# Performance work log

Measured on AMD Instinct MI355X. Metric: run time of the kernel, lower is better.

The kernel has to match this reference:

```python
import jax, jax.numpy as jnp
import numpy as np

VOCAB = 10000
EMB = 256
FILTERS = 256
KS = [2, 3, 4]
NUM_LABELS = 6
B, L = 4, 256


def _conv1d_same(x, w, b, k):
    # x: [B, C, L], w: [O, I, k] -> [B, O, L]; torch 'same' pad: left=(k-1)//2
    pad_l = (k - 1) // 2
    pad_r = (k - 1) - pad_l
    y = jax.lax.conv_general_dilated(
        x, w, window_strides=(1,), padding=[(pad_l, pad_r)],
        dimension_numbers=('NCH', 'OIH', 'NCH'))
    return y + b[None, :, None]


def setup_inputs() -> dict:
    key = jax.random.key(0)
    ks = jax.random.split(key, 12)
    s = 0.02
    return {
        'input_ids': jax.random.randint(ks[0], (B, L), 0, VOCAB),
        'emb_table': jax.random.normal(ks[1], (VOCAB, EMB), jnp.float32) * s,
        'w2': jax.random.normal(ks[2], (FILTERS, EMB, 2), jnp.float32) * s,
        'b2': jax.random.normal(ks[3], (FILTERS,), jnp.float32) * s,
        'w3': jax.random.normal(ks[4], (FILTERS, EMB, 3), jnp.float32) * s,
        'b3': jax.random.normal(ks[5], (FILTERS,), jnp.float32) * s,
        'w4': jax.random.normal(ks[6], (FILTERS, EMB, 4), jnp.float32) * s,
        'b4': jax.random.normal(ks[7], (FILTERS,), jnp.float32) * s,
        'triple_w': jax.random.normal(ks[8], (NUM_LABELS, 3 * FILTERS), jnp.float32) * s,
        'triple_b': jax.random.normal(ks[9], (NUM_LABELS,), jnp.float32) * s,
        'score_w': jax.random.normal(ks[10], (1, 3 * FILTERS), jnp.float32) * s,
        'score_b': jax.random.normal(ks[11], (1,), jnp.float32) * s,
    }


def reference(input_ids, emb_table, w2, b2, w3, b3, w4, b4,
              triple_w, triple_b, score_w, score_b):
    emb = emb_table[input_ids]              # [B, L, E]
    x = jnp.transpose(emb, (0, 2, 1))       # [B, E, L]
    outs = [_conv1d_same(x, w, b, k) for (w, b, k)
            in ((w2, b2, 2), (w3, b3, 3), (w4, b4, 4))]
    out = jnp.concatenate(outs, axis=1)     # [B, 3F, L]
    out = jnp.transpose(out, (0, 2, 1))     # [B, L, K], K = 3F
    # dropout is identity in eval mode
    pair = jnp.einsum('bik,bjk->bijk', out, out)          # [B, L, L, K]
    triple_logits = jnp.einsum('bijk,ck->bijc', pair, triple_w) + triple_b
    scores = jnp.einsum('bijk,ck->bijc', pair, score_w) + score_b
    scores = scores[..., 0]                 # squeeze(-1) -> [B, L, L]
    return triple_logits, scores
```

## Files before the change

kernel.cpp:

```cpp
#include <hip/hip_runtime.h>
#include <stdint.h>

#define LSEQ 256
#define EMB  256
#define K3F  768
#define SCOFF (4 * 256 * 256 * 6)

typedef short bf16x8 __attribute__((ext_vector_type(8)));
typedef float f32x4  __attribute__((ext_vector_type(4)));

__device__ __forceinline__ uint16_t f2bf(float x) {
    union { float f; uint32_t u; } c; c.f = x;
    uint32_t r = c.u + 0x7fffu + ((c.u >> 16) & 1u);
    return (uint16_t)(r >> 16);
}

__global__ __launch_bounds__(256) void k_prep(const int* __restrict__ ids,
                                              const float* __restrict__ table,
                                              const float* __restrict__ w2,
                                              const float* __restrict__ w3,
                                              const float* __restrict__ w4,
                                              uint16_t* __restrict__ embB,
                                              uint16_t* __restrict__ Wt2,
                                              uint16_t* __restrict__ Wt3,
                                              uint16_t* __restrict__ Wt4) {
    int blk = blockIdx.x, tid = threadIdx.x;
    if (blk < 32) {
        int b = blk >> 3, l0 = (blk & 7) << 5;
        int r = tid >> 3, p = tid & 7;
        int id = ids[(b << 8) + l0 + r];
        const float* src = table + (size_t)id * EMB + p * 32;
        uint16_t* dst = embB + (size_t)(b * 272 + 4 + l0 + r) * 256 + p * 32;
#pragma unroll
        for (int s = 0; s < 8; ++s) {
            float4 v = *(const float4*)(src + 4 * s);
            uint32_t lo = f2bf(v.x) | ((uint32_t)f2bf(v.y) << 16);
            uint32_t hi = f2bf(v.z) | ((uint32_t)f2bf(v.w) << 16);
            *(uint2*)(dst + 4 * s) = make_uint2(lo, hi);
        }
    } else if (blk < 36) {
        int b = blk - 32;
        int ri = tid >> 4;
        int row = ri < 4 ? ri : 256 + ri;
        int off = (tid & 15) * 16;
        uint16_t* dst = embB + (size_t)(b * 272 + row) * 256 + off;
        *(uint4*)dst = make_uint4(0, 0, 0, 0);
        *(uint4*)(dst + 8) = make_uint4(0, 0, 0, 0);
    } else {
        int n = (blk - 36) * 256 + tid;
        if (n < 65536) {
            int c = n >> 8, i = n & 255;
            float2 v = *(const float2*)(w2 + (c << 9) + (i << 1));
            Wt2[c * 256 + i]         = f2bf(v.x);
            Wt2[65536 + c * 256 + i] = f2bf(v.y);
        } else if (n < 131072) {
            int m = n - 65536;
            int c = m >> 8, i = m & 255;
            const float* s = w3 + c * 768 + i * 3;
#pragma unroll
            for (int t = 0; t < 3; ++t)
                Wt3[t * 65536 + c * 256 + i] = f2bf(s[t]);
        } else {
            int m = n - 131072;
            int c = m >> 8, i = m & 255;
            float4 v = *(const float4*)(w4 + (c << 10) + (i << 2));
            Wt4[c * 256 + i]              = f2bf(v.x);
            Wt4[65536 + c * 256 + i]      = f2bf(v.y);
            Wt4[2 * 65536 + c * 256 + i]  = f2bf(v.z);
            Wt4[3 * 65536 + c * 256 + i]  = f2bf(v.w);
        }
    }
}

template <int K, int PAD>
__device__ __forceinline__ void convg_body(const uint16_t* __restrict__ Wt,
                                           const float* __restrict__ bias,
                                           const uint16_t* __restrict__ embB,
                                           const float* __restrict__ tw,
                                           const float* __restrict__ sw,
                                           uint16_t* __restrict__ VB,
                                           uint16_t* __restrict__ U,
                                           int b, int c0, int l0, int gbase,
                                           uint16_t (*As)[32][72], uint16_t (*Bs)[72],
                                           float (*twb)[32]) {
    const int tid = threadIdx.x;
    {
        int cm = tid >> 5, cc = tid & 31;
        int gch = gbase + c0 + cc;
        float v;
        if (cm < 6) v = tw[cm * K3F + gch];
        else if (cm == 6) v = sw[gch];
        else v = bias[c0 + cc];
        twb[cm][cc] = v;
    }
    const int lane = tid & 63, wave = tid >> 6;
    const int ms = wave >> 1, ns = wave & 1;
    const int m = lane & 15, q = lane >> 4;
    const int ar = tid >> 3, aseg = (tid & 7) * 8;

    f32x4 acc;
#pragma unroll
    for (int z = 0; z < 4; ++z) acc[z] = 0.f;

    for (int i0 = 0; i0 < EMB; i0 += 64) {
        __syncthreads();
#pragma unroll
        for (int t = 0; t < K; ++t) {
            const uint16_t* src = Wt + (size_t)((t * 256 + c0 + ar) * 256 + i0) + aseg;
            *(bf16x8*)&As[t][ar][aseg] = *(const bf16x8*)src;
        }
        {
            const uint16_t* src = embB + (size_t)(b * 272 + 3 + l0 + ar) * 256 + i0 + aseg;
            *(bf16x8*)&Bs[ar][aseg] = *(const bf16x8*)src;
            if (tid < 32) {
                int r2 = 32 + (tid >> 3);
                const uint16_t* s2 = embB + (size_t)(b * 272 + 3 + l0 + r2) * 256 + i0 + aseg;
                *(bf16x8*)&Bs[r2][aseg] = *(const bf16x8*)s2;
            }
        }
        __syncthreads();
#pragma unroll
        for (int t = 0; t < K; ++t) {
#pragma unroll
            for (int kh = 0; kh < 64; kh += 32) {
                bf16x8 afr = *(const bf16x8*)&As[t][ms * 16 + m][kh + q * 8];
                bf16x8 bfr = *(const bf16x8*)&Bs[ns * 16 + m + t - PAD + 1][kh + q * 8];
                acc = __builtin_amdgcn_mfma_f32_16x16x32_bf16(afr, bfr, acc, 0, 0, 0);
            }
        }
    }
    __syncthreads();
    float (*Cs)[36] = (float(*)[36])As;
#pragma unroll
    for (int rg = 0; rg < 4; ++rg)
        Cs[ms * 16 + q * 4 + rg][ns * 16 + m] = acc[rg];
    __syncthreads();
    const int l = tid >> 3, cs = (tid & 7) * 4;
    float vals[4];
#pragma unroll
    for (int v = 0; v < 4; ++v) vals[v] = Cs[cs + v][l] + twb[7][cs + v];
    union { uint16_t h[4]; uint32_t d[2]; } pk;
#pragma unroll
    for (int v = 0; v < 4; ++v) pk.h[v] = f2bf(vals[v]);
    uint16_t* vdst = VB + (size_t)(b * 256 + l0 + l) * K3F + gbase + c0 + cs;
    *(uint2*)vdst = *(const uint2*)pk.d;
#pragma unroll
    for (int cm = 0; cm < 7; ++cm) {
#pragma unroll
        for (int v = 0; v < 4; ++v) pk.h[v] = f2bf(vals[v] * twb[cm][cs + v]);
        uint16_t* udst = U + (size_t)((b * 7 + cm) * 256 + l0 + l) * K3F + gbase + c0 + cs;
        *(uint2*)udst = *(const uint2*)pk.d;
    }
}

__global__ __launch_bounds__(256, 2) void k_convg(const uint16_t* __restrict__ Wt2,
                                                  const uint16_t* __restrict__ Wt3,
                                                  const uint16_t* __restrict__ Wt4,
                                                  const float* __restrict__ b2,
                                                  const float* __restrict__ b3,
                                                  const float* __restrict__ b4,
                                                  const uint16_t* __restrict__ embB,
                                                  const float* __restrict__ tw,
                                                  const float* __restrict__ sw,
                                                  uint16_t* __restrict__ VB,
                                                  uint16_t* __restrict__ U) {
    __shared__ uint16_t As[4][32][72];
    __shared__ uint16_t Bs[36][72];
    __shared__ float twb[8][32];
    int blk = blockIdx.x;
    int b = blk & 3, rest = blk >> 2;
    int g = rest >> 6, rr = rest & 63;
    int c0 = (rr >> 3) * 32, l0 = (rr & 7) * 32;
    if (g == 0)      convg_body<2, 0>(Wt2, b2, embB, tw, sw, VB, U, b, c0, l0, 0,   As, Bs, twb);
    else if (g == 1) convg_body<3, 1>(Wt3, b3, embB, tw, sw, VB, U, b, c0, l0, 256, As, Bs, twb);
    else             convg_body<4, 1>(Wt4, b4, embB, tw, sw, VB, U, b, c0, l0, 512, As, Bs, twb);
}

__global__ __launch_bounds__(256, 4) void k_pairc2(const uint16_t* __restrict__ U,
                                                   const uint16_t* __restrict__ VB,
                                                   const float* __restrict__ tb,
                                                   const float* __restrict__ sb,
                                                   float* __restrict__ dout) {
    __shared__ uint16_t T[96][136];
    int blk = blockIdx.x;
    int b = blk & 3, it = (blk >> 2) & 7;
    int rest = blk >> 5;
    int c = rest % 7, jp = rest / 7;
    int i0 = it * 32, j0 = jp * 64;
    int tid = threadIdx.x;
    int lane = tid & 63, wave = tid >> 6;
    int iw = wave >> 1, jw = wave & 1;
    int m = lane & 15, q = lane >> 4;
    int rr = tid >> 3, seg = (tid & 7) * 16;

    const uint16_t* srcp[3];
    srcp[0] = U + (size_t)((b * 7 + c) * 256 + i0 + rr) * K3F + seg;
    srcp[1] = VB + (size_t)(b * 256 + j0 + rr) * K3F + seg;
    srcp[2] = VB + (size_t)(b * 256 + j0 + 32 + rr) * K3F + seg;

    f32x4 acc[2];
#pragma unroll
    for (int n = 0; n < 2; ++n)
#pragma unroll
        for (int z = 0; z < 4; ++z) acc[n][z] = 0.f;

    for (int kc = 0; kc < K3F; kc += 128) {
        __syncthreads();
#pragma unroll
        for (int p = 0; p < 3; ++p) {
            const uint16_t* s = srcp[p] + kc;
            *(bf16x8*)&T[p * 32 + rr][seg]     = *(const bf16x8*)s;
            *(bf16x8*)&T[p * 32 + rr][seg + 8] = *(const bf16x8*)(s + 8);
        }
        __syncthreads();
#pragma unroll
        for (int kh = 0; kh < 4; ++kh) {
            bf16x8 afr  = *(const bf16x8*)&T[iw * 16 + m][kh * 32 + q * 8];
            bf16x8 bfr0 = *(const bf16x8*)&T[32 + jw * 32 + m][kh * 32 + q * 8];
            bf16x8 bfr1 = *(const bf16x8*)&T[32 + jw * 32 + 16 + m][kh * 32 + q * 8];
            acc[0] = __builtin_amdgcn_mfma_f32_16x16x32_bf16(afr, bfr0, acc[0], 0, 0, 0);
            acc[1] = __builtin_amdgcn_mfma_f32_16x16x32_bf16(afr, bfr1, acc[1], 0, 0, 0);
        }
    }
    float bias = (c < 6) ? tb[c] : sb[0];
#pragma unroll
    for (int n = 0; n < 2; ++n)
#pragma unroll
        for (int rg = 0; rg < 4; ++rg) {
            int i = i0 + iw * 16 + q * 4 + rg;
            int j = j0 + jw * 32 + n * 16 + m;
            float v = acc[n][rg] + bias;
            if (c < 6) dout[((size_t)(b * 256 + i) * 256 + j) * 6 + c] = v;
            else       dout[SCOFF + (size_t)(b * 256 + i) * 256 + j] = v;
        }
}

extern "C" void kernel_launch(void* const* d_in, const int* in_sizes, int n_in,
                              void* d_out, int out_size, void* d_ws, size_t ws_size,
                              hipStream_t stream) {
    const int*   ids   = (const int*)d_in[0];
    const float* table = (const float*)d_in[1];
    const float* w2 = (const float*)d_in[2];
    const float* b2 = (const float*)d_in[3];
    const float* w3 = (const float*)d_in[4];
    const float* b3 = (const float*)d_in[5];
    const float* w4 = (const float*)d_in[6];
    const float* b4 = (const float*)d_in[7];
    const float* tw = (const float*)d_in[8];
    const float* tb = (const float*)d_in[9];
    const float* sw = (const float*)d_in[10];
    const float* sb = (const float*)d_in[11];
    float* dout = (float*)d_out;

    uint8_t* wsb = (uint8_t*)d_ws;
    uint16_t* VB   = (uint16_t*)(wsb + 0);
    uint16_t* U    = (uint16_t*)(wsb + 1572864);
    uint16_t* embB = (uint16_t*)(wsb + 12582912);
    uint16_t* Wt2  = (uint16_t*)(wsb + 13139968);
    uint16_t* Wt3  = (uint16_t*)(wsb + 13402112);
    uint16_t* Wt4  = (uint16_t*)(wsb + 13795328);

    hipLaunchKernelGGL(k_prep,   dim3(804), dim3(256), 0, stream,
                       ids, table, w2, w3, w4, embB, Wt2, Wt3, Wt4);
    hipLaunchKernelGGL(k_convg,  dim3(768), dim3(256), 0, stream,
                       Wt2, Wt3, Wt4, b2, b3, b4, embB, tw, sw, VB, U);
    hipLaunchKernelGGL(k_pairc2, dim3(896), dim3(256), 0, stream, U, VB, tb, sb, dout);
}
```

Before: 109.3 us.

## Fuse weight scaling into pair GEMM operand load instead of materializing U

The conv kernel no longer writes the seven weight-scaled copies of the conv output (U, about 11 MB of bf16). Instead the pair kernel reads VB rows and multiplies them by the triple/score weights while staging the A tile into shared memory. This removes a large global write and the matching read, and in exchange adds per-tile float conversions and extra fp32 weight loads in the pair kernel. The staging layout for the B operand changes to four 16-byte loads per thread over 64 rows.

```diff
diff --git a/kernel.cpp b/kernel.cpp
--- a/kernel.cpp
+++ b/kernel.cpp
@@ -13,6 +13,12 @@
     union { float f; uint32_t u; } c; c.f = x;
     uint32_t r = c.u + 0x7fffu + ((c.u >> 16) & 1u);
     return (uint16_t)(r >> 16);
+}
+__device__ __forceinline__ float bfhi(uint32_t u) {
+    union { uint32_t u; float f; } c; c.u = u & 0xffff0000u; return c.f;
+}
+__device__ __forceinline__ float bflo(uint32_t u) {
+    union { uint32_t u; float f; } c; c.u = u << 16; return c.f;
 }
 
 __global__ __launch_bounds__(256) void k_prep(const int* __restrict__ ids,
@@ -76,23 +82,12 @@
 __device__ __forceinline__ void convg_body(const uint16_t* __restrict__ Wt,
                                            const float* __restrict__ bias,
                                            const uint16_t* __restrict__ embB,
-                                           const float* __restrict__ tw,
-                                           const float* __restrict__ sw,
                                            uint16_t* __restrict__ VB,
-                                           uint16_t* __restrict__ U,
                                            int b, int c0, int l0, int gbase,
                                            uint16_t (*As)[32][72], uint16_t (*Bs)[72],
-                                           float (*twb)[32]) {
+                                           float* bs) {
     const int tid = threadIdx.x;
-    {
-        int cm = tid >> 5, cc = tid & 31;
-        int gch = gbase + c0 + cc;
-        float v;
-        if (cm < 6) v = tw[cm * K3F + gch];
-        else if (cm == 6) v = sw[gch];
-        else v = bias[c0 + cc];
-        twb[cm][cc] = v;
-    }
+    if (tid < 32) bs[tid] = bias[c0 + tid];
     const int lane = tid & 63, wave = tid >> 6;
     const int ms = wave >> 1, ns = wave & 1;
     const int m = lane & 15, q = lane >> 4;
@@ -136,21 +131,11 @@
         Cs[ms * 16 + q * 4 + rg][ns * 16 + m] = acc[rg];
     __syncthreads();
     const int l = tid >> 3, cs = (tid & 7) * 4;
-    float vals[4];
-#pragma unroll
-    for (int v = 0; v < 4; ++v) vals[v] = Cs[cs + v][l] + twb[7][cs + v];
     union { uint16_t h[4]; uint32_t d[2]; } pk;
 #pragma unroll
-    for (int v = 0; v < 4; ++v) pk.h[v] = f2bf(vals[v]);
+    for (int v = 0; v < 4; ++v) pk.h[v] = f2bf(Cs[cs + v][l] + bs[cs + v]);
     uint16_t* vdst = VB + (size_t)(b * 256 + l0 + l) * K3F + gbase + c0 + cs;
     *(uint2*)vdst = *(const uint2*)pk.d;
-#pragma unroll
-    for (int cm = 0; cm < 7; ++cm) {
-#pragma unroll
-        for (int v = 0; v < 4; ++v) pk.h[v] = f2bf(vals[v] * twb[cm][cs + v]);
-        uint16_t* udst = U + (size_t)((b * 7 + cm) * 256 + l0 + l) * K3F + gbase + c0 + cs;
-        *(uint2*)udst = *(const uint2*)pk.d;
-    }
 }
 
 __global__ __launch_bounds__(256, 2) void k_convg(const uint16_t* __restrict__ Wt2,
@@ -160,24 +145,22 @@
                                                   const float* __restrict__ b3,
                                                   const float* __restrict__ b4,
                                                   const uint16_t* __restrict__ embB,
-                                                  const float* __restrict__ tw,
-                                                  const float* __restrict__ sw,
-                                                  uint16_t* __restrict__ VB,
-                                                  uint16_t* __restrict__ U) {
+                                                  uint16_t* __restrict__ VB) {
     __shared__ uint16_t As[4][32][72];
     __shared__ uint16_t Bs[36][72];
-    __shared__ float twb[8][32];
+    __shared__ float bs[32];
     int blk = blockIdx.x;
     int b = blk & 3, rest = blk >> 2;
     int g = rest >> 6, rr = rest & 63;
     int c0 = (rr >> 3) * 32, l0 = (rr & 7) * 32;
-    if (g == 0)      convg_body<2, 0>(Wt2, b2, embB, tw, sw, VB, U, b, c0, l0, 0,   As, Bs, twb);
-    else if (g == 1) convg_body<3, 1>(Wt3, b3, embB, tw, sw, VB, U, b, c0, l0, 256, As, Bs, twb);
-    else             convg_body<4, 1>(Wt4, b4, embB, tw, sw, VB, U, b, c0, l0, 512, As, Bs, twb);
-}
-
-__global__ __launch_bounds__(256, 4) void k_pairc2(const uint16_t* __restrict__ U,
-                                                   const uint16_t* __restrict__ VB,
+    if (g == 0)      convg_body<2, 0>(Wt2, b2, embB, VB, b, c0, l0, 0,   As, Bs, bs);
+    else if (g == 1) convg_body<3, 1>(Wt3, b3, embB, VB, b, c0, l0, 256, As, Bs, bs);
+    else             convg_body<4, 1>(Wt4, b4, embB, VB, b, c0, l0, 512, As, Bs, bs);
+}
+
+__global__ __launch_bounds__(256, 4) void k_pairc3(const uint16_t* __restrict__ VB,
+                                                   const float* __restrict__ tw,
+                                                   const float* __restrict__ sw,
                                                    const float* __restrict__ tb,
                                                    const float* __restrict__ sb,
                                                    float* __restrict__ dout) {
@@ -191,12 +174,12 @@
     int lane = tid & 63, wave = tid >> 6;
     int iw = wave >> 1, jw = wave & 1;
     int m = lane & 15, q = lane >> 4;
-    int rr = tid >> 3, seg = (tid & 7) * 16;
-
-    const uint16_t* srcp[3];
-    srcp[0] = U + (size_t)((b * 7 + c) * 256 + i0 + rr) * K3F + seg;
-    srcp[1] = VB + (size_t)(b * 256 + j0 + rr) * K3F + seg;
-    srcp[2] = VB + (size_t)(b * 256 + j0 + 32 + rr) * K3F + seg;
+
+    const float* twp = (c < 6) ? tw + c * K3F : sw;
+    const int ra = tid >> 3, sa = (tid & 7) * 16;
+    const int rb = tid >> 2, sb2 = (tid & 3) * 32;
+    const uint16_t* srcA = VB + (size_t)(b * 256 + i0 + ra) * K3F + sa;
+    const uint16_t* srcB = VB + (size_t)(b * 256 + j0 + rb) * K3F + sb2;
 
     f32x4 acc[2];
 #pragma unroll
@@ -206,11 +189,30 @@
 
     for (int kc = 0; kc < K3F; kc += 128) {
         __syncthreads();
-#pragma unroll
-        for (int p = 0; p < 3; ++p) {
-            const uint16_t* s = srcp[p] + kc;
-            *(bf16x8*)&T[p * 32 + rr][seg]     = *(const bf16x8*)s;
-            *(bf16x8*)&T[p * 32 + rr][seg + 8] = *(const bf16x8*)(s + 8);
+        {
+            uint4 a0 = *(const uint4*)(srcA + kc);
+            uint4 a1 = *(const uint4*)(srcA + kc + 8);
+            const float* tp = twp + kc + sa;
+            float4 t0 = *(const float4*)tp, t1 = *(const float4*)(tp + 4);
+            float4 t2 = *(const float4*)(tp + 8), t3 = *(const float4*)(tp + 12);
+            uint32_t o[8];
+            o[0] = f2bf(bflo(a0.x) * t0.x) | ((uint32_t)f2bf(bfhi(a0.x) * t0.y) << 16);
+            o[1] = f2bf(bflo(a0.y) * t0.z) | ((uint32_t)f2bf(bfhi(a0.y) * t0.w) << 16);
+            o[2] = f2bf(bflo(a0.z) * t1.x) | ((uint32_t)f2bf(bfhi(a0.z) * t1.y) << 16);
+            o[3] = f2bf(bflo(a0.w) * t1.z) | ((uint32_t)f2bf(bfhi(a0.w) * t1.w) << 16);
+            o[4] = f2bf(bflo(a1.x) * t2.x) | ((uint32_t)f2bf(bfhi(a1.x) * t2.y) << 16);
+            o[5] = f2bf(bflo(a1.y) * t2.z) | ((uint32_t)f2bf(bfhi(a1.y) * t2.w) << 16);
+            o[6] = f2bf(bflo(a1.z) * t3.x) | ((uint32_t)f2bf(bfhi(a1.z) * t3.y) << 16);
+            o[7] = f2bf(bflo(a1.w) * t3.z) | ((uint32_t)f2bf(bfhi(a1.w) * t3.w) << 16);
+            *(uint4*)&T[ra][sa]     = make_uint4(o[0], o[1], o[2], o[3]);
+            *(uint4*)&T[ra][sa + 8] = make_uint4(o[4], o[5], o[6], o[7]);
+        }
+        {
+            const uint16_t* s = srcB + kc;
+            *(bf16x8*)&T[32 + rb][sb2]      = *(const bf16x8*)s;
+            *(bf16x8*)&T[32 + rb][sb2 + 8]  = *(const bf16x8*)(s + 8);
+            *(bf16x8*)&T[32 + rb][sb2 + 16] = *(const bf16x8*)(s + 16);
+            *(bf16x8*)&T[32 + rb][sb2 + 24] = *(const bf16x8*)(s + 24);
         }
         __syncthreads();
 #pragma unroll
@@ -254,15 +256,15 @@
 
     uint8_t* wsb = (uint8_t*)d_ws;
     uint16_t* VB   = (uint16_t*)(wsb + 0);
-    uint16_t* U    = (uint16_t*)(wsb + 1572864);
-    uint16_t* embB = (uint16_t*)(wsb + 12582912);
-    uint16_t* Wt2  = (uint16_t*)(wsb + 13139968);
-    uint16_t* Wt3  = (uint16_t*)(wsb + 13402112);
-    uint16_t* Wt4  = (uint16_t*)(wsb + 13795328);
+    uint16_t* embB = (uint16_t*)(wsb + 1572864);
+    uint16_t* Wt2  = (uint16_t*)(wsb + 2129920);
+    uint16_t* Wt3  = (uint16_t*)(wsb + 2392064);
+    uint16_t* Wt4  = (uint16_t*)(wsb + 2785280);
 
     hipLaunchKernelGGL(k_prep,   dim3(804), dim3(256), 0, stream,
                        ids, table, w2, w3, w4, embB, Wt2, Wt3, Wt4);
     hipLaunchKernelGGL(k_convg,  dim3(768), dim3(256), 0, stream,
-                       Wt2, Wt3, Wt4, b2, b3, b4, embB, tw, sw, VB, U);
-    hipLaunchKernelGGL(k_pairc2, dim3(896), dim3(256), 0, stream, U, VB, tb, sb, dout);
-}
+                       Wt2, Wt3, Wt4, b2, b3, b4, embB, VB);
+    hipLaunchKernelGGL(k_pairc3, dim3(896), dim3(256), 0, stream,
+                       VB, tw, sw, tb, sb, dout);
+}
```

Result: slower. 112.1 us (+2.5%).
